# Optimization experiments

Measured on AMD Instinct MI355X. Metric: run time of the kernel, lower is better.

Reference implementation:

```python
import jax, jax.numpy as jnp
import numpy as np

EPS = 1e-5
TOP_K = 2


def setup_inputs() -> dict:
    key = jax.random.key(0)
    ks = jax.random.split(key, 8)
    B, T, D, E, F = 4, 2048, 1024, 8, 4096
    s_in = 1.0 / np.sqrt(D)
    s_ff = 1.0 / np.sqrt(F)
    return {
        "hidden_states": jax.random.normal(ks[0], (B, T, D), jnp.float32),
        "input_tensor": jax.random.normal(ks[1], (B, T, D), jnp.float32),
        "gate_w": jax.random.normal(ks[2], (D, E), jnp.float32) * s_in,
        "gate_b": jnp.zeros((E,), jnp.float32),
        "w1": jax.random.normal(ks[3], (E, D, F), jnp.float32) * s_in,
        "b1": jnp.zeros((E, F), jnp.float32),
        "w2": jax.random.normal(ks[4], (E, F, D), jnp.float32) * s_ff,
        "b2": jnp.zeros((E, D), jnp.float32),
        "gamma": jnp.ones((D,), jnp.float32),
        "beta": jnp.zeros((D,), jnp.float32),
    }


def _layer_norm(x, gamma, beta):
    mu = jnp.mean(x, axis=-1, keepdims=True)
    var = jnp.mean(jnp.square(x - mu), axis=-1, keepdims=True)
    return (x - mu) * jax.lax.rsqrt(var + EPS) * gamma + beta


def reference(hidden_states, input_tensor, gate_w, gate_b, w1, b1, w2, b2, gamma, beta):
    E = gate_b.shape[0]
    # Router: softmax over experts, then top-k gate values/indices.
    gate_logits = jnp.einsum("btd,de->bte", hidden_states, gate_w) + gate_b
    gate_probs = jax.nn.softmax(gate_logits, axis=-1)
    topk_gates, topk_idx = jax.lax.top_k(gate_probs, TOP_K)  # [B,T,K]
    # Combine weights per expert: sum of top-k gate values routed to expert e.
    combine_w = jnp.sum(
        jax.nn.one_hot(topk_idx, E, dtype=hidden_states.dtype)
        * topk_gates[..., None],
        axis=-2,
    )  # [B,T,E]
    # Dispatch/combine: weighted sum of expert FFN outputs (loop over small fixed E).
    expert_outputs = jnp.zeros_like(hidden_states)
    for e in range(E):
        h = jax.nn.gelu(jnp.einsum("btd,df->btf", hidden_states, w1[e]) + b1[e])
        y = jnp.einsum("btf,fd->btd", h, w2[e]) + b2[e]
        expert_outputs = expert_outputs + combine_w[..., e:e + 1] * y
    # Dropout is identity in eval mode.
    return _layer_norm(expert_outputs + input_tensor, gamma, beta)
```

## Files before the change

kernel.cpp:

```cpp
#include <hip/hip_runtime.h>

#define TOKENS 8192
#define DIM 1024
#define NEXP 8
#define FDIM 4096

typedef __bf16 bf16x8 __attribute__((ext_vector_type(8)));
typedef float f32x4 __attribute__((ext_vector_type(4)));

__device__ __forceinline__ unsigned short f2bf(float f) {
  unsigned u = __builtin_bit_cast(unsigned, f);
  u += 0x7fffu + ((u >> 16) & 1u);
  return (unsigned short)(u >> 16);
}

__device__ __forceinline__ float bf2f(unsigned short s) {
  unsigned u = (unsigned)s << 16;
  return __builtin_bit_cast(float, u);
}

__device__ __forceinline__ void gload16(const void* g, void* l) {
  __builtin_amdgcn_global_load_lds(
      (const __attribute__((address_space(1))) unsigned int*)g,
      (__attribute__((address_space(3))) unsigned int*)l, 16, 0, 0);
}

__global__ void zero_counts_kernel(int* counts) {
  if (threadIdx.x < NEXP) counts[threadIdx.x] = 0;
}

__global__ void scan_kernel(const int* counts, int* offs) {
  if (threadIdx.x == 0) {
    int s = 0;
    for (int e = 0; e < NEXP; ++e) { offs[e] = s; s += counts[e]; }
    offs[NEXP] = s;
  }
}

__global__ void router_kernel(const float* __restrict__ hs,
                              const float* __restrict__ gw,
                              const float* __restrict__ gb,
                              int* __restrict__ counts,
                              int* __restrict__ tok_idx,
                              float* __restrict__ tok_w,
                              unsigned int* __restrict__ slotinfo,
                              unsigned short* __restrict__ hs_bf) {
  const int lane = threadIdx.x & 63;
  const int wid = threadIdx.x >> 6;
  const int t = blockIdx.x * 4 + wid;
  const float* row = hs + (size_t)t * DIM;

  float x[16];
  const float4* r4 = (const float4*)(row + lane * 16);
#pragma unroll
  for (int i = 0; i < 4; ++i) {
    float4 v = r4[i];
    x[i * 4 + 0] = v.x; x[i * 4 + 1] = v.y; x[i * 4 + 2] = v.z; x[i * 4 + 3] = v.w;
  }

  float acc[8];
#pragma unroll
  for (int e = 0; e < 8; ++e) acc[e] = 0.f;
#pragma unroll
  for (int i = 0; i < 16; ++i) {
    const int d = lane * 16 + i;
    const float4* g4 = (const float4*)(gw + (size_t)d * 8);
    float4 g0 = g4[0], g1 = g4[1];
    const float xv = x[i];
    acc[0] += xv * g0.x; acc[1] += xv * g0.y; acc[2] += xv * g0.z; acc[3] += xv * g0.w;
    acc[4] += xv * g1.x; acc[5] += xv * g1.y; acc[6] += xv * g1.z; acc[7] += xv * g1.w;
  }
#pragma unroll
  for (int sh = 1; sh < 64; sh <<= 1) {
#pragma unroll
    for (int e = 0; e < 8; ++e) acc[e] += __shfl_xor(acc[e], sh, 64);
  }
#pragma unroll
  for (int e = 0; e < 8; ++e) acc[e] += gb[e];

  float mx = acc[0];
#pragma unroll
  for (int e = 1; e < 8; ++e) mx = fmaxf(mx, acc[e]);
  float p[8];
  float sum = 0.f;
#pragma unroll
  for (int e = 0; e < 8; ++e) { p[e] = __expf(acc[e] - mx); sum += p[e]; }
  const float inv = 1.0f / sum;

  int i0 = 0; float b0 = p[0];
#pragma unroll
  for (int e = 1; e < 8; ++e) if (p[e] > b0) { b0 = p[e]; i0 = e; }
  int i1 = -1; float b1v = -1.f;
#pragma unroll
  for (int e = 0; e < 8; ++e) if (e != i0 && p[e] > b1v) { b1v = p[e]; i1 = e; }

  if (lane == 0) {
    int pos0 = atomicAdd(&counts[i0], 1);
    tok_idx[i0 * TOKENS + pos0] = t;
    tok_w[i0 * TOKENS + pos0] = b0 * inv;
    slotinfo[t * 2 + 0] = ((unsigned)i0 << 13) | (unsigned)pos0;
    int pos1 = atomicAdd(&counts[i1], 1);
    tok_idx[i1 * TOKENS + pos1] = t;
    tok_w[i1 * TOKENS + pos1] = b1v * inv;
    slotinfo[t * 2 + 1] = ((unsigned)i1 << 13) | (unsigned)pos1;
  }

  unsigned short us[16];
#pragma unroll
  for (int i = 0; i < 16; ++i) us[i] = f2bf(x[i]);
  uint4 o0, o1;
  o0.x = (unsigned)us[0] | ((unsigned)us[1] << 16);
  o0.y = (unsigned)us[2] | ((unsigned)us[3] << 16);
  o0.z = (unsigned)us[4] | ((unsigned)us[5] << 16);
  o0.w = (unsigned)us[6] | ((unsigned)us[7] << 16);
  o1.x = (unsigned)us[8] | ((unsigned)us[9] << 16);
  o1.y = (unsigned)us[10] | ((unsigned)us[11] << 16);
  o1.z = (unsigned)us[12] | ((unsigned)us[13] << 16);
  o1.w = (unsigned)us[14] | ((unsigned)us[15] << 16);
  uint4* dst = (uint4*)(hs_bf + (size_t)t * DIM + lane * 16);
  dst[0] = o0;
  dst[1] = o1;
}

__global__ void cast_transpose_kernel(const float* __restrict__ src,
                                      unsigned short* __restrict__ dst,
                                      int R, int C) {
  __shared__ float tile[64][65];
  const int e = blockIdx.z;
  const int r0 = blockIdx.y * 64;
  const int c0 = blockIdx.x * 64;
  const float* s = src + (size_t)e * R * C;
  unsigned int* d = (unsigned int*)(dst + (size_t)e * R * C);

#pragma unroll
  for (int i = 0; i < 16; ++i) {
    const int idx = threadIdx.x + i * 256;
    const int r = idx >> 6;
    const int c = idx & 63;
    tile[r][c] = s[(size_t)(r0 + r) * C + (c0 + c)];
  }
  __syncthreads();
#pragma unroll
  for (int i = 0; i < 8; ++i) {
    const int idx = threadIdx.x + i * 256;
    const int c = idx >> 5;
    const int r = (idx & 31) * 2;
    unsigned pk = (unsigned)f2bf(tile[r][c]) | ((unsigned)f2bf(tile[r + 1][c]) << 16);
    d[((size_t)(c0 + c) * R + (r0 + r)) >> 1] = pk;
  }
}


#define GEMM_KTILE(sb, sbW, DO_ISSUE, ...)                                          \
  {                                                                                 \
    bf16x8 a0_[4], b0_[4];                                                          \
    _Pragma("unroll") for (int f_ = 0; f_ < 4; ++f_)                                \
      a0_[f_] = *(const bf16x8*)(sm + (sb) + aoff[f_]);                             \
    _Pragma("unroll") for (int g_ = 0; g_ < 4; ++g_)                                \
      b0_[g_] = *(const bf16x8*)(sm + 65536 + (sb) + boff[g_]);                     \
    if (DO_ISSUE) {                                                                 \
      gload16(aS0, sm + (sbW) + wdst);                                              \
      gload16(aS1, sm + (sbW) + 8192 + wdst);                                       \
      aS0 += 64; aS1 += 64;                                                         \
    }                                                                               \
    __builtin_amdgcn_sched_barrier(0);                                              \
    __builtin_amdgcn_s_barrier();                                                   \
    asm volatile("s_waitcnt lgkmcnt(0)" ::: "memory");                              \
    __builtin_amdgcn_sched_barrier(0);                                              \
    __builtin_amdgcn_s_setprio(1);                                                  \
    _Pragma("unroll") for (int f_ = 0; f_ < 4; ++f_)                                \
      _Pragma("unroll") for (int g_ = 0; g_ < 4; ++g_)                              \
        acc[f_][g_] = __builtin_amdgcn_mfma_f32_16x16x32_bf16(                      \
            a0_[f_], b0_[g_], acc[f_][g_], 0, 0, 0);                                \
    __builtin_amdgcn_s_setprio(0);                                                  \
    __builtin_amdgcn_sched_barrier(0);                                              \
    __builtin_amdgcn_s_barrier();                                                   \
    bf16x8 a1_[4];                                                                  \
    _Pragma("unroll") for (int f_ = 0; f_ < 4; ++f_)                                \
      a1_[f_] = *(const bf16x8*)(sm + (sb) + aoff[4 + f_]);                         \
    if (DO_ISSUE) {                                                                 \
      gload16(bS0, sm + 65536 + (sbW) + wdst);                                      \
      gload16(bS1, sm + 65536 + (sbW) + 8192 + wdst);                               \
      bS0 += 64; bS1 += 64;                                                         \
    }                                                                               \
    __VA_ARGS__;                                                                    \
    __builtin_amdgcn_sched_barrier(0);                                              \
    __builtin_amdgcn_s_barrier();                                                   \
    asm volatile("s_waitcnt lgkmcnt(0)" ::: "memory");                              \
    __builtin_amdgcn_sched_barrier(0);                                              \
    __builtin_amdgcn_s_setprio(1);                                                  \
    _Pragma("unroll") for (int f_ = 0; f_ < 4; ++f_)                                \
      _Pragma("unroll") for (int g_ = 0; g_ < 4; ++g_)                              \
        acc[4 + f_][g_] = __builtin_amdgcn_mfma_f32_16x16x32_bf16(                  \
            a1_[f_], b0_[g_], acc[4 + f_][g_], 0, 0, 0);                            \
    __builtin_amdgcn_s_setprio(0);                                                  \
    __builtin_amdgcn_sched_barrier(0);                                              \
    __builtin_amdgcn_s_barrier();                                                   \
  }

template<int MODE, int K, int N>
__global__ __launch_bounds__(512, 2)
void moe_gemm(const unsigned short* __restrict__ Abase,
              const unsigned short* __restrict__ Bbase,
              const float* __restrict__ bias,
              const int* __restrict__ counts,
              const int* __restrict__ offs,
              const int* __restrict__ tok_idx,
              unsigned short* __restrict__ dst) {
  constexpr int NT = K / 32;
  __shared__ __align__(16) unsigned char sm[131072];

  const int e = blockIdx.z;
  const int cnt = counts[e];
  const int m0 = blockIdx.y * 256;
  if (m0 >= cnt) return;
  const int n0 = blockIdx.x * 256;
  const int goff = offs[e];

  const int tid = threadIdx.x;
  const int lane = tid & 63;
  const int wid = tid >> 6;
  const int wr = wid >> 2;
  const int wcn = wid & 3;
  const int l15 = lane & 15;
  const int cg = lane >> 4;
  const int wdst = wid * 1024;

  const int urow = tid >> 2;
  const int uchk = tid & 3;
  const int swz = uchk ^ ((urow >> 1) & 3);
  const unsigned char* Bexp = (const unsigned char*)(Bbase + (size_t)e * K * N);

  int gA0 = m0 + urow;       if (gA0 > cnt - 1) gA0 = cnt - 1;
  int gA1 = m0 + urow + 128; if (gA1 > cnt - 1) gA1 = cnt - 1;
  size_t rowA0, rowA1;
  if (MODE == 0) {
    rowA0 = (size_t)tok_idx[e * TOKENS + gA0] * K;
    rowA1 = (size_t)tok_idx[e * TOKENS + gA1] * K;
  } else {
    rowA0 = (size_t)(goff + gA0) * K;
    rowA1 = (size_t)(goff + gA1) * K;
  }
  const unsigned char* aS0 = (const unsigned char*)(Abase + rowA0) + swz * 16;
  const unsigned char* aS1 = (const unsigned char*)(Abase + rowA1) + swz * 16;
  const unsigned char* bS0 = Bexp + (size_t)(n0 + urow) * (K * 2) + swz * 16;
  const unsigned char* bS1 = Bexp + (size_t)(n0 + urow + 128) * (K * 2) + swz * 16;

  int aoff[8], boff[4];
#pragma unroll
  for (int f = 0; f < 8; ++f) {
    const int r = wr * 128 + f * 16 + l15;
    aoff[f] = r * 64 + ((cg ^ ((r >> 1) & 3)) * 16);
  }
#pragma unroll
  for (int g = 0; g < 4; ++g) {
    const int r = wcn * 64 + g * 16 + l15;
    boff[g] = r * 64 + ((cg ^ ((r >> 1) & 3)) * 16);
  }

  f32x4 acc[8][4];
  const f32x4 fz = {0.f, 0.f, 0.f, 0.f};
#pragma unroll
  for (int f = 0; f < 8; ++f)
#pragma unroll
    for (int g = 0; g < 4; ++g) acc[f][g] = fz;

#pragma unroll
  for (int j = 0; j < 3; ++j) {
    gload16(aS0, sm + j * 16384 + wdst);
    gload16(aS1, sm + j * 16384 + 8192 + wdst);
    gload16(bS0, sm + 65536 + j * 16384 + wdst);
    gload16(bS1, sm + 65536 + j * 16384 + 8192 + wdst);
    aS0 += 64; aS1 += 64; bS0 += 64; bS1 += 64;
  }
  asm volatile("s_waitcnt vmcnt(8)" ::: "memory");
  __builtin_amdgcn_sched_barrier(0);
  __builtin_amdgcn_s_barrier();

#pragma unroll 1
  for (int t = 0; t < NT - 3; ++t) {
    const int sb = (t & 3) * 16384;
    const int sbW = ((t + 3) & 3) * 16384;
    GEMM_KTILE(sb, sbW, true, asm volatile("s_waitcnt vmcnt(8)" ::: "memory"));
  }
  GEMM_KTILE(((NT - 3) & 3) * 16384, 0, false,
             asm volatile("s_waitcnt vmcnt(4)" ::: "memory"));
  GEMM_KTILE(((NT - 2) & 3) * 16384, 0, false,
             asm volatile("s_waitcnt vmcnt(0)" ::: "memory"));
  GEMM_KTILE(((NT - 1) & 3) * 16384, 0, false, ((void)0));

#pragma unroll
  for (int g = 0; g < 4; ++g) {
    const int fcol = n0 + wcn * 64 + g * 16 + l15;
    const float bv = bias[e * N + fcol];
#pragma unroll
    for (int f = 0; f < 8; ++f) {
#pragma unroll
      for (int j = 0; j < 4; ++j) {
        const int ml = wr * 128 + f * 16 + cg * 4 + j;
        const int gm = m0 + ml;
        if (gm < cnt) {
          float v = acc[f][g][j] + bv;
          if (MODE == 0) {
            const float u = 0.7978845608028654f * (v + 0.044715f * v * v * v);
            const float th = 1.0f - 2.0f / (1.0f + __expf(2.0f * u));
            v = 0.5f * v * (1.0f + th);
          }
          dst[(size_t)(goff + gm) * N + fcol] = f2bf(v);
        }
      }
    }
  }
}

__global__ void ln_combine_kernel(const unsigned short* __restrict__ y_buf,
                                  const float* __restrict__ in_t,
                                  const int* __restrict__ offs,
                                  const unsigned int* __restrict__ slotinfo,
                                  const float* __restrict__ tok_w,
                                  const float* __restrict__ gamma,
                                  const float* __restrict__ beta,
                                  float* __restrict__ out) {
  const int lane = threadIdx.x & 63;
  const int wid = threadIdx.x >> 6;
  const int t = blockIdx.x * 4 + wid;

  const unsigned s0 = slotinfo[t * 2 + 0];
  const unsigned s1 = slotinfo[t * 2 + 1];
  const int e0 = s0 >> 13, p0 = s0 & 8191;
  const int e1 = s1 >> 13, p1 = s1 & 8191;
  const float w0 = tok_w[e0 * TOKENS + p0];
  const float w1 = tok_w[e1 * TOKENS + p1];
  const size_t r0 = (size_t)(offs[e0] + p0) * DIM;
  const size_t r1 = (size_t)(offs[e1] + p1) * DIM;

  float v[16];
  {
    const float4* i4 = (const float4*)(in_t + (size_t)t * DIM + lane * 16);
    const uint4* y0 = (const uint4*)(y_buf + r0 + lane * 16);
    const uint4* y1 = (const uint4*)(y_buf + r1 + lane * 16);
#pragma unroll
    for (int i = 0; i < 4; ++i) {
      float4 a = i4[i];
      v[i * 4 + 0] = a.x; v[i * 4 + 1] = a.y; v[i * 4 + 2] = a.z; v[i * 4 + 3] = a.w;
    }
#pragma unroll
    for (int i = 0; i < 2; ++i) {
      uint4 u0 = y0[i];
      uint4 u1 = y1[i];
      const unsigned uw0[4] = {u0.x, u0.y, u0.z, u0.w};
      const unsigned uw1[4] = {u1.x, u1.y, u1.z, u1.w};
#pragma unroll
      for (int k = 0; k < 4; ++k) {
        const int base = i * 8 + k * 2;
        v[base + 0] += w0 * bf2f((unsigned short)(uw0[k] & 0xffff)) +
                       w1 * bf2f((unsigned short)(uw1[k] & 0xffff));
        v[base + 1] += w0 * bf2f((unsigned short)(uw0[k] >> 16)) +
                       w1 * bf2f((unsigned short)(uw1[k] >> 16));
      }
    }
  }

  float s = 0.f, s2 = 0.f;
#pragma unroll
  for (int i = 0; i < 16; ++i) { s += v[i]; s2 += v[i] * v[i]; }
#pragma unroll
  for (int sh = 1; sh < 64; sh <<= 1) {
    s += __shfl_xor(s, sh, 64);
    s2 += __shfl_xor(s2, sh, 64);
  }
  const float mu = s * (1.0f / DIM);
  const float var = s2 * (1.0f / DIM) - mu * mu;
  const float rs = rsqrtf(var + 1e-5f);

  float4* w4 = (float4*)(out + (size_t)t * DIM + lane * 16);
#pragma unroll
  for (int i = 0; i < 4; ++i) {
    const int d = lane * 16 + i * 4;
    float4 g = *(const float4*)(gamma + d);
    float4 b = *(const float4*)(beta + d);
    float4 o;
    o.x = (v[i * 4 + 0] - mu) * rs * g.x + b.x;
    o.y = (v[i * 4 + 1] - mu) * rs * g.y + b.y;
    o.z = (v[i * 4 + 2] - mu) * rs * g.z + b.z;
    o.w = (v[i * 4 + 3] - mu) * rs * g.w + b.w;
    w4[i] = o;
  }
}

extern "C" void kernel_launch(void* const* d_in, const int* in_sizes, int n_in,
                              void* d_out, int out_size, void* d_ws, size_t ws_size,
                              hipStream_t stream) {
  const float* hs    = (const float*)d_in[0];
  const float* in_t  = (const float*)d_in[1];
  const float* gw    = (const float*)d_in[2];
  const float* gb    = (const float*)d_in[3];
  const float* w1    = (const float*)d_in[4];
  const float* b1    = (const float*)d_in[5];
  const float* w2    = (const float*)d_in[6];
  const float* b2    = (const float*)d_in[7];
  const float* gamma = (const float*)d_in[8];
  const float* beta  = (const float*)d_in[9];
  float* out = (float*)d_out;
  char* ws = (char*)d_ws;

  int* counts            = (int*)(ws + 0);
  int* offs              = (int*)(ws + 256);
  unsigned int* slotinfo = (unsigned int*)(ws + 512);
  int* tok_idx           = (int*)(ws + 66048);
  float* tok_w           = (float*)(ws + 328192);
  unsigned short* hs_bf  = (unsigned short*)(ws + 590336);
  unsigned short* w1t    = (unsigned short*)(ws + 17367552);
  unsigned short* w2t    = (unsigned short*)(ws + 84476416);
  unsigned short* h_buf  = (unsigned short*)(ws + 151585280);
  unsigned short* y_buf  = (unsigned short*)(ws + 590336);

  zero_counts_kernel<<<1, 64, 0, stream>>>(counts);
  router_kernel<<<TOKENS / 4, 256, 0, stream>>>(hs, gw, gb, counts, tok_idx, tok_w,
                                                slotinfo, hs_bf);
  scan_kernel<<<1, 64, 0, stream>>>(counts, offs);
  cast_transpose_kernel<<<dim3(FDIM / 64, DIM / 64, NEXP), 256, 0, stream>>>(w1, w1t, DIM, FDIM);
  cast_transpose_kernel<<<dim3(DIM / 64, FDIM / 64, NEXP), 256, 0, stream>>>(w2, w2t, FDIM, DIM);
  moe_gemm<0, DIM, FDIM><<<dim3(FDIM / 256, TOKENS / 256, NEXP), 512, 0, stream>>>(
      hs_bf, w1t, b1, counts, offs, tok_idx, h_buf);
  moe_gemm<1, FDIM, DIM><<<dim3(DIM / 256, TOKENS / 256, NEXP), 512, 0, stream>>>(
      h_buf, w2t, b2, counts, offs, tok_idx, y_buf);
  ln_combine_kernel<<<TOKENS / 4, 256, 0, stream>>>(y_buf, in_t, offs, slotinfo,
                                                    tok_w, gamma, beta, out);
}
```

Before: 798.3 us.

## Prefetch next k-tile fragments across barrier and halve barriers per k-tile

```diff
diff --git a/kernel.cpp b/kernel.cpp
--- a/kernel.cpp
+++ b/kernel.cpp
@@ -151,51 +151,47 @@
 }
 
 
-#define GEMM_KTILE(sb, sbW, DO_ISSUE, ...)                                          \
-  {                                                                                 \
-    bf16x8 a0_[4], b0_[4];                                                          \
-    _Pragma("unroll") for (int f_ = 0; f_ < 4; ++f_)                                \
-      a0_[f_] = *(const bf16x8*)(sm + (sb) + aoff[f_]);                             \
-    _Pragma("unroll") for (int g_ = 0; g_ < 4; ++g_)                                \
-      b0_[g_] = *(const bf16x8*)(sm + 65536 + (sb) + boff[g_]);                     \
-    if (DO_ISSUE) {                                                                 \
-      gload16(aS0, sm + (sbW) + wdst);                                              \
-      gload16(aS1, sm + (sbW) + 8192 + wdst);                                       \
-      aS0 += 64; aS1 += 64;                                                         \
-    }                                                                               \
-    __builtin_amdgcn_sched_barrier(0);                                              \
-    __builtin_amdgcn_s_barrier();                                                   \
-    asm volatile("s_waitcnt lgkmcnt(0)" ::: "memory");                              \
-    __builtin_amdgcn_sched_barrier(0);                                              \
-    __builtin_amdgcn_s_setprio(1);                                                  \
-    _Pragma("unroll") for (int f_ = 0; f_ < 4; ++f_)                                \
-      _Pragma("unroll") for (int g_ = 0; g_ < 4; ++g_)                              \
-        acc[f_][g_] = __builtin_amdgcn_mfma_f32_16x16x32_bf16(                      \
-            a0_[f_], b0_[g_], acc[f_][g_], 0, 0, 0);                                \
-    __builtin_amdgcn_s_setprio(0);                                                  \
-    __builtin_amdgcn_sched_barrier(0);                                              \
-    __builtin_amdgcn_s_barrier();                                                   \
-    bf16x8 a1_[4];                                                                  \
-    _Pragma("unroll") for (int f_ = 0; f_ < 4; ++f_)                                \
-      a1_[f_] = *(const bf16x8*)(sm + (sb) + aoff[4 + f_]);                         \
-    if (DO_ISSUE) {                                                                 \
-      gload16(bS0, sm + 65536 + (sbW) + wdst);                                      \
-      gload16(bS1, sm + 65536 + (sbW) + 8192 + wdst);                               \
-      bS0 += 64; bS1 += 64;                                                         \
-    }                                                                               \
-    __VA_ARGS__;                                                                    \
-    __builtin_amdgcn_sched_barrier(0);                                              \
-    __builtin_amdgcn_s_barrier();                                                   \
-    asm volatile("s_waitcnt lgkmcnt(0)" ::: "memory");                              \
-    __builtin_amdgcn_sched_barrier(0);                                              \
-    __builtin_amdgcn_s_setprio(1);                                                  \
-    _Pragma("unroll") for (int f_ = 0; f_ < 4; ++f_)                                \
-      _Pragma("unroll") for (int g_ = 0; g_ < 4; ++g_)                              \
-        acc[4 + f_][g_] = __builtin_amdgcn_mfma_f32_16x16x32_bf16(                  \
-            a1_[f_], b0_[g_], acc[4 + f_][g_], 0, 0, 0);                            \
-    __builtin_amdgcn_s_setprio(0);                                                  \
-    __builtin_amdgcn_sched_barrier(0);                                              \
-    __builtin_amdgcn_s_barrier();                                                   \
+#define DO_TILE(sTp, sNp, A0C, B0C, A0N, B0N, STA, STB, WSA, GATESTR, READN, FINAL)   \
+  {                                                                                   \
+    bf16x8 a1r[4];                                                                    \
+    _Pragma("unroll") for (int f_ = 0; f_ < 4; ++f_)                                  \
+      a1r[f_] = *(const bf16x8*)((sTp) + aoff[4 + f_]);                               \
+    if (STA) {                                                                        \
+      gload16(aS0, (WSA));                                                            \
+      gload16(aS1, (WSA) + 8192);                                                     \
+      aS0 += 64; aS1 += 64;                                                           \
+    }                                                                                 \
+    __builtin_amdgcn_sched_barrier(0);                                                \
+    __builtin_amdgcn_s_setprio(1);                                                    \
+    _Pragma("unroll") for (int f_ = 0; f_ < 4; ++f_)                                  \
+      _Pragma("unroll") for (int g_ = 0; g_ < 4; ++g_)                                \
+        acc[f_][g_] = __builtin_amdgcn_mfma_f32_16x16x32_bf16(                        \
+            A0C[f_], B0C[g_], acc[f_][g_], 0, 0, 0);                                  \
+    __builtin_amdgcn_s_setprio(0);                                                    \
+    __builtin_amdgcn_sched_barrier(0);                                                \
+    if (!(FINAL)) {                                                                   \
+      asm volatile(GATESTR ::: "memory");                                             \
+      __builtin_amdgcn_s_barrier();                                                   \
+    }                                                                                 \
+    if (READN) {                                                                      \
+      _Pragma("unroll") for (int f_ = 0; f_ < 4; ++f_)                                \
+        A0N[f_] = *(const bf16x8*)((sNp) + aoff[f_]);                                 \
+      _Pragma("unroll") for (int g_ = 0; g_ < 4; ++g_)                                \
+        B0N[g_] = *(const bf16x8*)((sNp) + 65536 + boff[g_]);                         \
+    }                                                                                 \
+    if (STB) {                                                                        \
+      gload16(bS0, (WSA) + 65536);                                                    \
+      gload16(bS1, (WSA) + 65536 + 8192);                                             \
+      bS0 += 64; bS1 += 64;                                                           \
+    }                                                                                 \
+    __builtin_amdgcn_sched_barrier(0);                                                \
+    __builtin_amdgcn_s_setprio(1);                                                    \
+    _Pragma("unroll") for (int f_ = 0; f_ < 4; ++f_)                                  \
+      _Pragma("unroll") for (int g_ = 0; g_ < 4; ++g_)                                \
+        acc[4 + f_][g_] = __builtin_amdgcn_mfma_f32_16x16x32_bf16(                    \
+            a1r[f_], B0C[g_], acc[4 + f_][g_], 0, 0, 0);                              \
+    __builtin_amdgcn_s_setprio(0);                                                    \
+    __builtin_amdgcn_sched_barrier(0);                                                \
   }
 
 template<int MODE, int K, int N>
@@ -268,26 +264,51 @@
 #pragma unroll
   for (int j = 0; j < 3; ++j) {
     gload16(aS0, sm + j * 16384 + wdst);
-    gload16(aS1, sm + j * 16384 + 8192 + wdst);
+    gload16(aS1, sm + j * 16384 + wdst + 8192);
+    aS0 += 64; aS1 += 64;
     gload16(bS0, sm + 65536 + j * 16384 + wdst);
-    gload16(bS1, sm + 65536 + j * 16384 + 8192 + wdst);
-    aS0 += 64; aS1 += 64; bS0 += 64; bS1 += 64;
+    gload16(bS1, sm + 65536 + j * 16384 + wdst + 8192);
+    bS0 += 64; bS1 += 64;
   }
   asm volatile("s_waitcnt vmcnt(8)" ::: "memory");
   __builtin_amdgcn_sched_barrier(0);
   __builtin_amdgcn_s_barrier();
 
+  const unsigned char* smc = (const unsigned char*)sm;
+  bf16x8 a0A[4], b0A[4], a0B[4], b0B[4];
+#pragma unroll
+  for (int f = 0; f < 4; ++f) a0A[f] = *(const bf16x8*)(smc + aoff[f]);
+#pragma unroll
+  for (int g = 0; g < 4; ++g) b0A[g] = *(const bf16x8*)(smc + 65536 + boff[g]);
+
+  int t = 0;
 #pragma unroll 1
-  for (int t = 0; t < NT - 3; ++t) {
-    const int sb = (t & 3) * 16384;
-    const int sbW = ((t + 3) & 3) * 16384;
-    GEMM_KTILE(sb, sbW, true, asm volatile("s_waitcnt vmcnt(8)" ::: "memory"));
-  }
-  GEMM_KTILE(((NT - 3) & 3) * 16384, 0, false,
-             asm volatile("s_waitcnt vmcnt(4)" ::: "memory"));
-  GEMM_KTILE(((NT - 2) & 3) * 16384, 0, false,
-             asm volatile("s_waitcnt vmcnt(0)" ::: "memory"));
-  GEMM_KTILE(((NT - 1) & 3) * 16384, 0, false, ((void)0));
+  for (; t + 5 < NT; t += 2) {
+    const unsigned char* sT0 = smc + ((t & 3) << 14);
+    const unsigned char* sT1 = smc + (((t + 1) & 3) << 14);
+    const unsigned char* sT2 = smc + (((t + 2) & 3) << 14);
+    unsigned char* w3 = (unsigned char*)sm + (((t + 3) & 3) << 14) + wdst;
+    unsigned char* w4 = (unsigned char*)sm + (((t + 4) & 3) << 14) + wdst;
+    DO_TILE(sT0, sT1, a0A, b0A, a0B, b0B, 1, 1, w3,
+            "s_waitcnt vmcnt(6) lgkmcnt(0)", 1, 0);
+    DO_TILE(sT1, sT2, a0B, b0B, a0A, b0A, 1, 1, w4,
+            "s_waitcnt vmcnt(6) lgkmcnt(0)", 1, 0);
+  }
+  {
+    const unsigned char* sT0 = smc + ((t & 3) << 14);
+    const unsigned char* sT1 = smc + (((t + 1) & 3) << 14);
+    const unsigned char* sT2 = smc + (((t + 2) & 3) << 14);
+    const unsigned char* sT3 = smc + (((t + 3) & 3) << 14);
+    unsigned char* w3 = (unsigned char*)sm + (((t + 3) & 3) << 14) + wdst;
+    DO_TILE(sT0, sT1, a0A, b0A, a0B, b0B, 1, 1, w3,
+            "s_waitcnt vmcnt(6) lgkmcnt(0)", 1, 0);
+    DO_TILE(sT1, sT2, a0B, b0B, a0A, b0A, 0, 0, w3,
+            "s_waitcnt vmcnt(4) lgkmcnt(0)", 1, 0);
+    DO_TILE(sT2, sT3, a0A, b0A, a0B, b0B, 0, 0, w3,
+            "s_waitcnt vmcnt(0) lgkmcnt(0)", 1, 0);
+    DO_TILE(sT3, sT3, a0B, b0B, a0A, b0A, 0, 0, w3,
+            "", 0, 1);
+  }
 
 #pragma unroll
   for (int g = 0; g < 4; ++g) {
```

New measurement: 767.8 us. 1.04x faster.

## Load B operand directly to registers, halve LDS, and cut barriers per k-tile

Applied to the files above, without the earlier changes.

```diff
diff --git a/kernel.cpp b/kernel.cpp
--- a/kernel.cpp
+++ b/kernel.cpp
@@ -151,51 +151,48 @@
 }
 
 
-#define GEMM_KTILE(sb, sbW, DO_ISSUE, ...)                                          \
+#define MOE_TILE(SB, SNB, WB, BCUR, BNXT, A0C, A0N, DOA, DOB, GATE, DOGATE, READN)  \
   {                                                                                 \
-    bf16x8 a0_[4], b0_[4];                                                          \
+    bf16x8 a1r_[4];                                                                 \
     _Pragma("unroll") for (int f_ = 0; f_ < 4; ++f_)                                \
-      a0_[f_] = *(const bf16x8*)(sm + (sb) + aoff[f_]);                             \
-    _Pragma("unroll") for (int g_ = 0; g_ < 4; ++g_)                                \
-      b0_[g_] = *(const bf16x8*)(sm + 65536 + (sb) + boff[g_]);                     \
-    if (DO_ISSUE) {                                                                 \
-      gload16(aS0, sm + (sbW) + wdst);                                              \
-      gload16(aS1, sm + (sbW) + 8192 + wdst);                                       \
+      a1r_[f_] = *(const bf16x8*)((SB) + aoff[4 + f_]);                             \
+    if (DOA) {                                                                      \
+      gload16(aS0, (WB));                                                           \
+      gload16(aS1, (WB) + 8192);                                                    \
       aS0 += 64; aS1 += 64;                                                         \
     }                                                                               \
-    __builtin_amdgcn_sched_barrier(0);                                              \
-    __builtin_amdgcn_s_barrier();                                                   \
-    asm volatile("s_waitcnt lgkmcnt(0)" ::: "memory");                              \
+    if (DOB) {                                                                      \
+      _Pragma("unroll") for (int g_ = 0; g_ < 4; ++g_) {                            \
+        BNXT[g_] = *(const bf16x8*)bP[g_];                                          \
+        bP[g_] += 64;                                                               \
+      }                                                                             \
+    }                                                                               \
     __builtin_amdgcn_sched_barrier(0);                                              \
     __builtin_amdgcn_s_setprio(1);                                                  \
     _Pragma("unroll") for (int f_ = 0; f_ < 4; ++f_)                                \
       _Pragma("unroll") for (int g_ = 0; g_ < 4; ++g_)                              \
         acc[f_][g_] = __builtin_amdgcn_mfma_f32_16x16x32_bf16(                      \
-            a0_[f_], b0_[g_], acc[f_][g_], 0, 0, 0);                                \
+            A0C[f_], BCUR[g_], acc[f_][g_], 0, 0, 0);                               \
     __builtin_amdgcn_s_setprio(0);                                                  \
     __builtin_amdgcn_sched_barrier(0);                                              \
-    __builtin_amdgcn_s_barrier();                                                   \
-    bf16x8 a1_[4];                                                                  \
-    _Pragma("unroll") for (int f_ = 0; f_ < 4; ++f_)                                \
-      a1_[f_] = *(const bf16x8*)(sm + (sb) + aoff[4 + f_]);                         \
-    if (DO_ISSUE) {                                                                 \
-      gload16(bS0, sm + 65536 + (sbW) + wdst);                                      \
-      gload16(bS1, sm + 65536 + (sbW) + 8192 + wdst);                               \
-      bS0 += 64; bS1 += 64;                                                         \
+    if (DOGATE) {                                                                   \
+      asm volatile(GATE ::: "memory");                                              \
+      __builtin_amdgcn_sched_barrier(0);                                            \
+      __builtin_amdgcn_s_barrier();                                                 \
+      __builtin_amdgcn_sched_barrier(0);                                            \
     }                                                                               \
-    __VA_ARGS__;                                                                    \
-    __builtin_amdgcn_sched_barrier(0);                                              \
-    __builtin_amdgcn_s_barrier();                                                   \
-    asm volatile("s_waitcnt lgkmcnt(0)" ::: "memory");                              \
+    if (READN) {                                                                    \
+      _Pragma("unroll") for (int f_ = 0; f_ < 4; ++f_)                              \
+        A0N[f_] = *(const bf16x8*)((SNB) + aoff[f_]);                               \
+    }                                                                               \
     __builtin_amdgcn_sched_barrier(0);                                              \
     __builtin_amdgcn_s_setprio(1);                                                  \
     _Pragma("unroll") for (int f_ = 0; f_ < 4; ++f_)                                \
       _Pragma("unroll") for (int g_ = 0; g_ < 4; ++g_)                              \
         acc[4 + f_][g_] = __builtin_amdgcn_mfma_f32_16x16x32_bf16(                  \
-            a1_[f_], b0_[g_], acc[4 + f_][g_], 0, 0, 0);                            \
+            a1r_[f_], BCUR[g_], acc[4 + f_][g_], 0, 0, 0);                          \
     __builtin_amdgcn_s_setprio(0);                                                  \
     __builtin_amdgcn_sched_barrier(0);                                              \
-    __builtin_amdgcn_s_barrier();                                                   \
   }
 
 template<int MODE, int K, int N>
@@ -208,7 +205,7 @@
               const int* __restrict__ tok_idx,
               unsigned short* __restrict__ dst) {
   constexpr int NT = K / 32;
-  __shared__ __align__(16) unsigned char sm[131072];
+  __shared__ __align__(16) unsigned char sm[65536];
 
   const int e = blockIdx.z;
   const int cnt = counts[e];
@@ -229,7 +226,6 @@
   const int urow = tid >> 2;
   const int uchk = tid & 3;
   const int swz = uchk ^ ((urow >> 1) & 3);
-  const unsigned char* Bexp = (const unsigned char*)(Bbase + (size_t)e * K * N);
 
   int gA0 = m0 + urow;       if (gA0 > cnt - 1) gA0 = cnt - 1;
   int gA1 = m0 + urow + 128; if (gA1 > cnt - 1) gA1 = cnt - 1;
@@ -243,20 +239,19 @@
   }
   const unsigned char* aS0 = (const unsigned char*)(Abase + rowA0) + swz * 16;
   const unsigned char* aS1 = (const unsigned char*)(Abase + rowA1) + swz * 16;
-  const unsigned char* bS0 = Bexp + (size_t)(n0 + urow) * (K * 2) + swz * 16;
-  const unsigned char* bS1 = Bexp + (size_t)(n0 + urow + 128) * (K * 2) + swz * 16;
-
-  int aoff[8], boff[4];
+
+  const unsigned char* Bexp = (const unsigned char*)(Bbase + (size_t)e * K * N);
+  const unsigned char* bP[4];
+#pragma unroll
+  for (int g = 0; g < 4; ++g)
+    bP[g] = Bexp + (size_t)(n0 + wcn * 64 + g * 16 + l15) * (K * 2) + cg * 16;
+
+  int aoff[8];
 #pragma unroll
   for (int f = 0; f < 8; ++f) {
     const int r = wr * 128 + f * 16 + l15;
     aoff[f] = r * 64 + ((cg ^ ((r >> 1) & 3)) * 16);
   }
-#pragma unroll
-  for (int g = 0; g < 4; ++g) {
-    const int r = wcn * 64 + g * 16 + l15;
-    boff[g] = r * 64 + ((cg ^ ((r >> 1) & 3)) * 16);
-  }
 
   f32x4 acc[8][4];
   const f32x4 fz = {0.f, 0.f, 0.f, 0.f};
@@ -265,29 +260,51 @@
 #pragma unroll
     for (int g = 0; g < 4; ++g) acc[f][g] = fz;
 
+  bf16x8 BbA[4], BbB[4];
+  bf16x8 a0X[4], a0Y[4];
+
+#pragma unroll
+  for (int g = 0; g < 4; ++g) { BbA[g] = *(const bf16x8*)bP[g]; bP[g] += 64; }
 #pragma unroll
   for (int j = 0; j < 3; ++j) {
     gload16(aS0, sm + j * 16384 + wdst);
-    gload16(aS1, sm + j * 16384 + 8192 + wdst);
-    gload16(bS0, sm + 65536 + j * 16384 + wdst);
-    gload16(bS1, sm + 65536 + j * 16384 + 8192 + wdst);
-    aS0 += 64; aS1 += 64; bS0 += 64; bS1 += 64;
-  }
-  asm volatile("s_waitcnt vmcnt(8)" ::: "memory");
+    gload16(aS1, sm + j * 16384 + wdst + 8192);
+    aS0 += 64; aS1 += 64;
+  }
+  asm volatile("s_waitcnt vmcnt(4)" ::: "memory");
   __builtin_amdgcn_sched_barrier(0);
   __builtin_amdgcn_s_barrier();
 
+  const unsigned char* smc = (const unsigned char*)sm;
+#pragma unroll
+  for (int f = 0; f < 4; ++f) a0X[f] = *(const bf16x8*)(smc + aoff[f]);
+
+  const unsigned char* S0 = smc;
+  const unsigned char* S1 = smc + 16384;
+  const unsigned char* S2 = smc + 32768;
+  const unsigned char* S3 = smc + 49152;
+  unsigned char* W0 = (unsigned char*)sm + wdst;
+  unsigned char* W1 = (unsigned char*)sm + 16384 + wdst;
+  unsigned char* W2 = (unsigned char*)sm + 32768 + wdst;
+  unsigned char* W3 = (unsigned char*)sm + 49152 + wdst;
+
+  MOE_TILE(S0, S1, W3, BbA, BbB, a0X, a0Y, 1, 1, "s_waitcnt vmcnt(8) lgkmcnt(0)", 1, 1);
+  MOE_TILE(S1, S2, W0, BbB, BbA, a0Y, a0X, 1, 1, "s_waitcnt vmcnt(12) lgkmcnt(0)", 1, 1);
+  MOE_TILE(S2, S3, W1, BbA, BbB, a0X, a0Y, 1, 1, "s_waitcnt vmcnt(12) lgkmcnt(0)", 1, 1);
+  MOE_TILE(S3, S0, W2, BbB, BbA, a0Y, a0X, 1, 1, "s_waitcnt vmcnt(12) lgkmcnt(0)", 1, 1);
+
 #pragma unroll 1
-  for (int t = 0; t < NT - 3; ++t) {
-    const int sb = (t & 3) * 16384;
-    const int sbW = ((t + 3) & 3) * 16384;
-    GEMM_KTILE(sb, sbW, true, asm volatile("s_waitcnt vmcnt(8)" ::: "memory"));
-  }
-  GEMM_KTILE(((NT - 3) & 3) * 16384, 0, false,
-             asm volatile("s_waitcnt vmcnt(4)" ::: "memory"));
-  GEMM_KTILE(((NT - 2) & 3) * 16384, 0, false,
-             asm volatile("s_waitcnt vmcnt(0)" ::: "memory"));
-  GEMM_KTILE(((NT - 1) & 3) * 16384, 0, false, ((void)0));
+  for (int t = 4; t + 7 < NT; t += 4) {
+    MOE_TILE(S0, S1, W3, BbA, BbB, a0X, a0Y, 1, 1, "s_waitcnt vmcnt(12) lgkmcnt(0)", 1, 1);
+    MOE_TILE(S1, S2, W0, BbB, BbA, a0Y, a0X, 1, 1, "s_waitcnt vmcnt(12) lgkmcnt(0)", 1, 1);
+    MOE_TILE(S2, S3, W1, BbA, BbB, a0X, a0Y, 1, 1, "s_waitcnt vmcnt(12) lgkmcnt(0)", 1, 1);
+    MOE_TILE(S3, S0, W2, BbB, BbA, a0Y, a0X, 1, 1, "s_waitcnt vmcnt(12) lgkmcnt(0)", 1, 1);
+  }
+
+  MOE_TILE(S0, S1, W3, BbA, BbB, a0X, a0Y, 1, 1, "s_waitcnt vmcnt(12) lgkmcnt(0)", 1, 1);
+  MOE_TILE(S1, S2, W0, BbB, BbA, a0Y, a0X, 0, 1, "s_waitcnt vmcnt(12) lgkmcnt(0)", 1, 1);
+  MOE_TILE(S2, S3, W1, BbA, BbB, a0X, a0Y, 0, 1, "s_waitcnt vmcnt(12) lgkmcnt(0)", 1, 1);
+  MOE_TILE(S3, S0, W2, BbB, BbA, a0Y, a0X, 0, 0, "", 0, 0);
 
 #pragma unroll
   for (int g = 0; g < 4; ++g) {
```

New measurement: 1.020 ms. +27.8%, slower.
